# Kernel tuning notes

Hardware: AMD Instinct MI355X
Metric: run time of the kernel (lower is better)

The kernel has to match this reference:

```python
import jax, jax.numpy as jnp
import numpy as np

C = 256; COUT = 256; G = 8; GC = C // G; K = 3; P = K * K
PAD = 1; DIL = 1; STR = 1
EPS = 1e-5


def _group_norm(x, gamma, beta, groups=32, eps=EPS):
    # x: (N,H,W,C), torch.nn.GroupNorm semantics (biased var)
    N, H, W, Cc = x.shape
    xg = x.reshape(N, H, W, groups, Cc // groups)
    mu = xg.mean(axis=(1, 2, 4), keepdims=True)
    var = xg.var(axis=(1, 2, 4), keepdims=True)
    xg = (xg - mu) * jax.lax.rsqrt(var + eps)
    return xg.reshape(N, H, W, Cc) * gamma + beta


def _conv2d(x, w, b, stride=1, pad=1, groups=1):
    y = jax.lax.conv_general_dilated(
        x, w, (stride, stride), [(pad, pad), (pad, pad)],
        dimension_numbers=('NHWC', 'HWIO', 'NHWC'),
        feature_group_count=groups)
    return y + b


def _bilinear_gather(img, px, py, Hin, Win):
    x0 = jnp.floor(px); y0 = jnp.floor(py)
    wx1 = px - x0; wy1 = py - y0
    out = jnp.zeros(img.shape[:1] + px.shape[1:] + img.shape[-1:], img.dtype)
    for xi, wx in ((x0, 1.0 - wx1), (x0 + 1.0, wx1)):
        for yi, wy in ((y0, 1.0 - wy1), (y0 + 1.0, wy1)):
            valid = (xi >= 0) & (xi < Win) & (yi >= 0) & (yi < Hin)
            idx = (jnp.clip(yi, 0, Hin - 1) * Win + jnp.clip(xi, 0, Win - 1)).astype(jnp.int32)
            vals = jnp.take_along_axis(img, idx[..., None], axis=1)
            out = out + vals * (wx * wy * valid)[..., None]
    return out


def _forward(x, w_in, b_in, dw_w, dw_b, ln_g, ln_b, w_off, b_off, w_mask, b_mask,
             w_out, b_out, gn1_g, gn1_b, conv1_w, conv1_b, gn2_g, gn2_b,
             down_w, down_b, gn3_g, gn3_b):
    xs = jnp.transpose(x, (0, 2, 3, 1))  # NHWC
    N, H, W, _ = xs.shape
    # ---- DCNv3 ----
    x_proj = xs @ w_in + b_in                              # input_proj
    t = _conv2d(xs, dw_w, dw_b, stride=STR, pad=(K - 1) // 2, groups=C)  # depthwise
    mu = t.mean(-1, keepdims=True)
    var = t.var(-1, keepdims=True)
    t = (t - mu) * jax.lax.rsqrt(var + EPS) * ln_g + ln_b  # LayerNorm
    t = jax.nn.gelu(t, approximate=False)
    offset = (t @ w_off + b_off).reshape(N, H, W, G, P, 2)  # (x,y) pairs
    mask = jax.nn.softmax((t @ w_mask + b_mask).reshape(N, H, W, G, P), axis=-1)

    Hin, Win = H + 2 * PAD, W + 2 * PAD
    xp = jnp.pad(x_proj, ((0, 0), (PAD, PAD), (PAD, PAD), (0, 0)))
    base = (DIL * (K - 1)) // 2 + 0.5
    ref_y = (base + jnp.arange(H, dtype=xs.dtype) * STR) / Hin
    ref_x = (base + jnp.arange(W, dtype=xs.dtype) * STR) / Win
    ry, rx = jnp.meshgrid(ref_y, ref_x, indexing='ij')
    ref = jnp.stack([rx, ry], -1)[None, :, :, None, None, :]  # (1,H,W,1,1,2)
    d = jnp.arange(K, dtype=xs.dtype) * DIL - (DIL * (K - 1)) // 2
    gx, gy = jnp.meshgrid(d, d, indexing='ij')  # x varies fastest over axis0 (torch order)
    grid = jnp.stack([gx / Win, gy / Hin], -1).reshape(P, 2)
    spatial = jnp.array([Win, Hin], xs.dtype)
    loc = ref + grid + offset / spatial          # normalized [0,1], offset_scale=1
    px = loc[..., 0] * Win - 0.5                 # align_corners=False pixel coords
    py = loc[..., 1] * Hin - 0.5

    L = H * W
    img = xp.reshape(N, Hin * Win, G, GC).transpose(0, 2, 1, 3).reshape(N * G, Hin * Win, GC)
    pxf = jnp.transpose(px, (0, 3, 1, 2, 4)).reshape(N * G, L * P)
    pyf = jnp.transpose(py, (0, 3, 1, 2, 4)).reshape(N * G, L * P)
    sampled = _bilinear_gather(img, pxf, pyf, Hin, Win).reshape(N, G, L, P, GC)
    m = jnp.transpose(mask, (0, 3, 1, 2, 4)).reshape(N, G, L, P)
    agg = jnp.einsum('nglpc,nglp->nglc', sampled, m)
    y = agg.transpose(0, 2, 1, 3).reshape(N, H, W, C)
    y = y @ w_out + b_out                        # output_proj
    # ---- block_out ----
    y = jax.nn.silu(_group_norm(y, gn1_g, gn1_b))
    y = _conv2d(y, conv1_w, conv1_b, stride=1, pad=1)
    y = jax.nn.silu(_group_norm(y, gn2_g, gn2_b))
    # ---- down_sample ----
    y = _conv2d(y, down_w, down_b, stride=2, pad=1)
    y = _group_norm(y, gn3_g, gn3_b)
    return jnp.transpose(y, (0, 3, 1, 2))  # back to NCHW


def setup_inputs() -> dict:
    key = jax.random.key(0)
    ks = jax.random.split(key, 10)
    f = jnp.float32
    nrm = lambda k, shape, s: jax.random.normal(k, shape, dtype=f) * s
    N, H, W = 4, 64, 64
    return {
        'x': jax.random.normal(ks[0], (N, C, H, W), dtype=f),
        'w_in': nrm(ks[1], (C, C), 0.05), 'b_in': jnp.zeros((C,), f),
        'dw_w': nrm(ks[2], (K, K, 1, C), 0.1), 'dw_b': jnp.zeros((C,), f),
        'ln_g': jnp.ones((C,), f), 'ln_b': jnp.zeros((C,), f),
        'w_off': nrm(ks[3], (C, 2 * G * P), 0.02), 'b_off': nrm(ks[4], (2 * G * P,), 1.0),
        'w_mask': nrm(ks[5], (C, G * P), 0.02), 'b_mask': jnp.zeros((G * P,), f),
        'w_out': nrm(ks[6], (C, C), 0.05), 'b_out': jnp.zeros((C,), f),
        'gn1_g': jnp.ones((C,), f), 'gn1_b': jnp.zeros((C,), f),
        'conv1_w': nrm(ks[7], (3, 3, C, C), 0.02), 'conv1_b': jnp.zeros((C,), f),
        'gn2_g': jnp.ones((C,), f), 'gn2_b': jnp.zeros((C,), f),
        'down_w': nrm(ks[8], (3, 3, C, COUT), 0.02), 'down_b': jnp.zeros((COUT,), f),
        'gn3_g': jnp.ones((COUT,), f), 'gn3_b': jnp.zeros((COUT,), f),
    }


def reference(x, w_in, b_in, dw_w, dw_b, ln_g, ln_b, w_off, b_off, w_mask, b_mask,
              w_out, b_out, gn1_g, gn1_b, conv1_w, conv1_b, gn2_g, gn2_b,
              down_w, down_b, gn3_g, gn3_b):
    return _forward(x, w_in, b_in, dw_w, dw_b, ln_g, ln_b, w_off, b_off, w_mask,
                    b_mask, w_out, b_out, gn1_g, gn1_b, conv1_w, conv1_b,
                    gn2_g, gn2_b, down_w, down_b, gn3_g, gn3_b)
```

## Files before the change

### kernel.cpp

```cpp
#include <hip/hip_runtime.h>
#include <hip/hip_bf16.h>
#include <math.h>


typedef __attribute__((ext_vector_type(8))) short bf16x8;
typedef __attribute__((ext_vector_type(4))) float f32x4;

__device__ __forceinline__ float bf2f(unsigned short u){
  union { unsigned int i; float f; } v; v.i = ((unsigned int)u)<<16; return v.f;
}
__device__ __forceinline__ float blo(unsigned u){
  union { unsigned int i; float f; } v; v.i = u<<16; return v.f;
}
__device__ __forceinline__ float bhi(unsigned u){
  union { unsigned int i; float f; } v; v.i = u & 0xffff0000u; return v.f;
}
__device__ __forceinline__ unsigned short f2b(float f){
  __hip_bfloat16 h = __float2bfloat16(f);
  return *reinterpret_cast<unsigned short*>(&h);
}
__device__ __forceinline__ unsigned pk2(float lo, float hi){
  return (unsigned)f2b(lo) | ((unsigned)f2b(hi)<<16);
}

__device__ __forceinline__ void gload16(const void* g, void* l){
  auto gp = reinterpret_cast<const __attribute__((address_space(1))) uint32_t*>(
      reinterpret_cast<uintptr_t>(g));
  auto lp = reinterpret_cast<__attribute__((address_space(3))) uint32_t*>(
      reinterpret_cast<uintptr_t>(l));
  __builtin_amdgcn_global_load_lds(gp, lp, 16, 0, 0);
}

__global__ __launch_bounds__(256) void k_prep(
    const float* __restrict__ w_in, const float* __restrict__ w_out,
    const float* __restrict__ conv1_w, const float* __restrict__ down_w,
    const float* __restrict__ w_off, const float* __restrict__ w_mask,
    const float* __restrict__ b_off, const float* __restrict__ b_mask,
    __hip_bfloat16* __restrict__ w_inT, __hip_bfloat16* __restrict__ w_outT,
    __hip_bfloat16* __restrict__ c1T, __hip_bfloat16* __restrict__ dnT,
    __hip_bfloat16* __restrict__ w_omT, float* __restrict__ bias_om,
    float* __restrict__ stats, __hip_bfloat16* __restrict__ R3)
{
  int b = blockIdx.x;
  if (b < 160){
    __shared__ float tl[32][257];
    const float* W; __hip_bfloat16* WT; int Kd, kb;
    if (b < 8)      { W = w_in;    WT = w_inT;  Kd = 256;  kb = b; }
    else if (b <16) { W = w_out;   WT = w_outT; Kd = 256;  kb = b-8; }
    else if (b <88) { W = conv1_w; WT = c1T;    Kd = 2304; kb = b-16; }
    else            { W = down_w;  WT = dnT;    Kd = 2304; kb = b-88; }
    int k0 = kb*32;
    #pragma unroll
    for (int dk=0; dk<32; dk++) tl[dk][threadIdx.x] = W[(size_t)(k0+dk)*256 + threadIdx.x];
    __syncthreads();
    #pragma unroll
    for (int r=0; r<32; r++){
      int co = r*8 + (threadIdx.x>>5);
      int dk = threadIdx.x&31;
      WT[(size_t)co*Kd + k0 + dk] = __float2bfloat16(tl[dk][co]);
    }
  } else if (b < 416){
    int n = b - 160, k = threadIdx.x;
    float v = (n<144) ? w_off[(size_t)k*144 + n] : (n<216 ? w_mask[(size_t)k*72 + (n-144)] : 0.f);
    w_omT[(size_t)n*256 + k] = __float2bfloat16(v);
    if (k==0) bias_om[n] = (n<144) ? b_off[n] : (n<216 ? b_mask[n-144] : 0.f);
  } else if (b < 546){
    int gid = (b-416)*8 + (threadIdx.x>>5);
    if (gid >= 1040) return;
    int n = gid/260; int ci = gid - n*260;
    int r, c;
    if (ci < 66){ r = 0; c = ci; }
    else if (ci < 132){ r = 65; c = ci-66; }
    else { int q = ci-132; r = 1 + (q>>1); c = (q&1) ? 65 : 0; }
    uint4* p = (uint4*)(R3 + ((size_t)((n*66+r)*66+c))*256) + (threadIdx.x&31);
    *p = make_uint4(0,0,0,0);
  } else {
    stats[threadIdx.x] = 0.f;
    stats[256+threadIdx.x] = 0.f;
    stats[512+threadIdx.x] = 0.f;
  }
}

__global__ __launch_bounds__(256) void k_tr(const float* __restrict__ x, __hip_bfloat16* __restrict__ xs){
  __shared__ float tile[32][33];
  int n = blockIdx.z;
  int hw0 = blockIdx.x*32, c0 = blockIdx.y*32;
  int tx = threadIdx.x, ty = threadIdx.y;
  #pragma unroll
  for (int ii=0; ii<4; ii++){
    int ci = ty + ii*8;
    tile[ci][tx] = x[(size_t)(n*256 + c0+ci)*4096 + hw0 + tx];
  }
  __syncthreads();
  #pragma unroll
  for (int ii=0; ii<4; ii++){
    int hwi = ty + ii*8;
    xs[((size_t)n*4096 + hw0+hwi)*256 + c0 + tx] = __float2bfloat16(tile[tx][hwi]);
  }
}

template<int AMODE, int OMODE, int STRIDE, int KTOT, int NSHIFT>
__global__ __launch_bounds__(256) void k_mm(
    const __hip_bfloat16* __restrict__ A, const __hip_bfloat16* __restrict__ Bt,
    const float* __restrict__ bias, float* __restrict__ OF, __hip_bfloat16* __restrict__ OH,
    float* __restrict__ stats)
{
  constexpr int AROWS = 64;
  constexpr int MI = AROWS/32;
  constexpr int WROWS = AROWS/2;
  constexpr int JA = AROWS*128/4096;
  constexpr int BUFSZ = AROWS*128 + 16384;
  __shared__ uint4 lds4[2*BUFSZ/16];
  char* ldsc = (char*)lds4;
  const int tid = threadIdx.x;
  const int lane = tid & 63;
  const int wv = tid >> 6;
  const int wr = wv >> 1, wc = wv & 1;
  const int m0 = blockIdx.x * AROWS, n0 = blockIdx.y * 128;

  const int swz_s = ((tid >> 3) & 7) << 4;
  const int cby = ((tid & 7) << 4) ^ swz_s;
  const int kl = cby >> 1;
  int aoff[JA], boff[4];
  #pragma unroll
  for (int j=0;j<JA;j++){
    int row = j*32 + (tid>>3);
    if (AMODE==0){
      aoff[j] = (m0 + row) * KTOT + kl;
    } else {
      int m = m0 + row;
      int n, ho, wo;
      if (STRIDE==1){ n = m>>12; ho = (m>>6)&63; wo = m&63; }
      else          { n = m>>10; ho = (m>>5)&31; wo = m&31; }
      aoff[j] = ((n*66 + ho*STRIDE)*66 + wo*STRIDE)*256 + kl;
    }
  }
  #pragma unroll
  for (int j=0;j<4;j++) boff[j] = (n0 + j*32 + (tid>>3)) * KTOT + kl;
  char* ldsst = ldsc + wv*1024;

  const int fr = lane & 15;
  const int kb = (lane >> 4) << 4;
  const int swz_r = (fr & 7) << 4;
  int aRow[MI], bRow[4];
  #pragma unroll
  for (int i=0;i<MI;i++) aRow[i] = (wr*WROWS + i*16 + fr) * 128;
  #pragma unroll
  for (int i=0;i<4;i++)  bRow[i] = AROWS*128 + (wc*64 + i*16 + fr) * 128;
  int cb[2];
  cb[0] = kb ^ swz_r;
  cb[1] = (64 | kb) ^ swz_r;

  f32x4 acc[MI][4];
  #pragma unroll
  for (int mi=0;mi<MI;mi++)
    #pragma unroll
    for (int ni=0;ni<4;ni++)
      acc[mi][ni] = (f32x4){0.f,0.f,0.f,0.f};

  auto STAGE = [&](int buf, int t){
    const int k0 = t*64;
    int astep;
    if (AMODE==1){
      int tap = k0 >> 8;
      int kh = (tap>=6) ? 2 : (tap>=3 ? 1 : 0);
      int kw = tap - kh*3;
      astep = (kh*66 + kw)*256 + (k0 & 255);
    } else astep = k0;
    char* db = ldsst + buf*BUFSZ;
    #pragma unroll
    for (int j=0;j<JA;j++) gload16(A + aoff[j] + astep, db + j*4096);
    #pragma unroll
    for (int j=0;j<4;j++)  gload16(Bt + boff[j] + k0, db + AROWS*128 + j*4096);
  };

  constexpr int NT = KTOT / 64;
  STAGE(0, 0);
  __syncthreads();
  for (int t=0; t<NT; ++t){
    if (t+1 < NT) STAGE((t+1)&1, t+1);
    char* cbase = ldsc + (t&1)*BUFSZ;
    #pragma unroll
    for (int kk=0; kk<2; kk++){
      bf16x8 av[MI], bv[4];
      #pragma unroll
      for (int i=0;i<MI;i++) av[i] = *(const bf16x8*)(cbase + aRow[i] + cb[kk]);
      #pragma unroll
      for (int i=0;i<4;i++)  bv[i] = *(const bf16x8*)(cbase + bRow[i] + cb[kk]);
      #pragma unroll
      for (int mi=0;mi<MI;mi++)
        #pragma unroll
        for (int ni=0;ni<4;ni++)
          acc[mi][ni] = __builtin_amdgcn_mfma_f32_16x16x32_bf16(av[mi], bv[ni], acc[mi][ni], 0,0,0);
    }
    __syncthreads();
  }

  float bn[4];
  #pragma unroll
  for (int ni=0;ni<4;ni++) bn[ni] = bias[n0 + wc*64 + ni*16 + fr];
  float sni[4] = {0.f,0.f,0.f,0.f};
  float qni[4] = {0.f,0.f,0.f,0.f};
  #pragma unroll
  for (int mi=0;mi<MI;mi++){
    #pragma unroll
    for (int r=0;r<4;r++){
      int gr = m0 + wr*WROWS + mi*16 + (lane>>4)*4 + r;
      #pragma unroll
      for (int ni=0;ni<4;ni++){
        int gc = n0 + wc*64 + ni*16 + fr;
        float v = acc[mi][ni][r] + bn[ni];
        if (NSHIFT){ sni[ni] += v; qni[ni] += v*v; }
        if (OMODE==0){
          OF[(size_t)gr*256 + gc] = v;
        } else if (OMODE==1){
          int n = gr>>12, h = (gr>>6)&63, w = gr&63;
          OH[((size_t)((n*66)+(h+1))*66 + (w+1))*256 + gc] = __float2bfloat16(v);
        } else {
          if (gc < 216) OF[(size_t)gr*216 + gc] = v;
        }
      }
    }
  }
  if (NSHIFT){
    #pragma unroll
    for (int ni=0;ni<4;ni++){
      #pragma unroll
      for (int msk=16; msk<64; msk<<=1){
        sni[ni] += __shfl_xor(sni[ni], msk);
        qni[ni] += __shfl_xor(qni[ni], msk);
      }
      #pragma unroll
      for (int msk=1; msk<8; msk<<=1){
        sni[ni] += __shfl_xor(sni[ni], msk);
        qni[ni] += __shfl_xor(qni[ni], msk);
      }
    }
    float* ls = (float*)ldsc;
    if (tid < 32) ls[tid] = 0.f;
    __syncthreads();
    if ((lane & 7) == 0 && (lane & 48) == 0){
      int oct = (lane>>3) & 1;
      #pragma unroll
      for (int ni=0;ni<4;ni++){
        int idx = wc*8 + ni*2 + oct;
        atomicAdd(&ls[idx], sni[ni]);
        atomicAdd(&ls[16+idx], qni[ni]);
      }
    }
    __syncthreads();
    if (tid < 16){
      int gg = (m0>>NSHIFT)*32 + (n0>>3) + tid;
      atomicAdd(&stats[gg*2+0], ls[tid]);
      atomicAdd(&stats[gg*2+1], ls[16+tid]);
    }
  }
}

__global__ __launch_bounds__(256) void k_dwln(
    const __hip_bfloat16* __restrict__ xs, const float* __restrict__ dw_w, const float* __restrict__ dw_b,
    const float* __restrict__ ln_g, const float* __restrict__ ln_b, __hip_bfloat16* __restrict__ t)
{
  __shared__ float lw[9*256];
  __shared__ float lb[256], lg[256], lbt[256];
  int tid = threadIdx.x;
  #pragma unroll
  for (int p=0;p<9;p++) lw[p*256+tid] = dw_w[p*256+tid];
  lb[tid] = dw_b[tid]; lg[tid] = ln_g[tid]; lbt[tid] = ln_b[tid];
  __syncthreads();
  int posl = tid>>5, cg = tid&31, c0 = cg*8;
  int pos = blockIdx.x*8 + posl;
  int nb = pos>>12, h = (pos>>6)&63, w = pos&63;
  float v[8];
  #pragma unroll
  for (int k=0;k<8;k++) v[k] = lb[c0+k];
  #pragma unroll
  for (int kh=0;kh<3;kh++){
    int hin = h+kh-1;
    if (hin<0||hin>=64) continue;
    #pragma unroll
    for (int kw=0;kw<3;kw++){
      int win = w+kw-1;
      if (win<0||win>=64) continue;
      const unsigned short* xr = (const unsigned short*)xs + ((size_t)((nb*64+hin)*64+win))*256 + c0;
      uint4 u = *(const uint4*)xr;
      const float* wr = &lw[(kh*3+kw)*256 + c0];
      v[0] += blo(u.x)*wr[0]; v[1] += bhi(u.x)*wr[1];
      v[2] += blo(u.y)*wr[2]; v[3] += bhi(u.y)*wr[3];
      v[4] += blo(u.z)*wr[4]; v[5] += bhi(u.z)*wr[5];
      v[6] += blo(u.w)*wr[6]; v[7] += bhi(u.w)*wr[7];
    }
  }
  float s=0.f, s2=0.f;
  #pragma unroll
  for (int k=0;k<8;k++){ s += v[k]; s2 += v[k]*v[k]; }
  #pragma unroll
  for (int m=1;m<32;m<<=1){ s += __shfl_xor(s,m); s2 += __shfl_xor(s2,m); }
  float mu = s*(1.f/256.f);
  float var = s2*(1.f/256.f) - mu*mu;
  float rstd = rsqrtf(var + 1e-5f);
  float ge[8];
  #pragma unroll
  for (int k=0;k<8;k++){
    float xn = (v[k]-mu)*rstd*lg[c0+k] + lbt[c0+k];
    ge[k] = 0.5f*xn*(1.f + erff(xn*0.70710678118654752f));
  }
  uint4 o;
  o.x = pk2(ge[0],ge[1]); o.y = pk2(ge[2],ge[3]);
  o.z = pk2(ge[4],ge[5]); o.w = pk2(ge[6],ge[7]);
  *(uint4*)((unsigned short*)t + (size_t)pos*256 + c0) = o;
}

__global__ __launch_bounds__(256) void k_sample(
    const __hip_bfloat16* __restrict__ xp, const float* __restrict__ D, __hip_bfloat16* __restrict__ y)
{
  int tid = threadIdx.x;
  int pp = tid>>5;
  int g = (tid>>2)&7, li = tid&3;
  int pos = blockIdx.x*8 + pp;
  int nb = pos >> 12, h = (pos >> 6) & 63, w = pos & 63;
  const float* Dp = D + (size_t)pos*216;
  const float* offp = Dp + g*18;
  const float* mskp = Dp + 144 + g*9;
  float mr[9];
  #pragma unroll
  for (int p=0;p<9;p++) mr[p] = mskp[p];
  float mx = mr[0];
  #pragma unroll
  for (int p=1;p<9;p++) mx = fmaxf(mx, mr[p]);
  float ssum = 0.f;
  #pragma unroll
  for (int p=0;p<9;p++){ mr[p] = __expf(mr[p]-mx); ssum += mr[p]; }
  float rinv = 1.f/ssum;
  const unsigned short* img = (const unsigned short*)xp + (size_t)nb*4356*256 + g*32 + li*8;
  float a0=0,a1=0,a2=0,a3=0,a4=0,a5=0,a6=0,a7=0;
  #pragma unroll
  for (int p=0;p<9;p++){
    int di = p/3 - 1, dj = p%3 - 1;
    float2 off = *(const float2*)(offp + p*2);
    float px = (float)(w + 1 + di) + off.x;
    float py = (float)(h + 1 + dj) + off.y;
    float x0f = floorf(px), y0f = floorf(py);
    float wx1 = px - x0f, wy1 = py - y0f;
    float wx0 = 1.f - wx1, wy0 = 1.f - wy1;
    int x0 = (int)x0f, y0 = (int)y0f;
    float s0=0,s1=0,s2=0,s3=0,s4=0,s5=0,s6=0,s7=0;
    #pragma unroll
    for (int cy=0;cy<2;cy++){
      int yi = y0+cy;
      if (yi<0||yi>=66) continue;
      float wy = cy ? wy1 : wy0;
      #pragma unroll
      for (int cx=0;cx<2;cx++){
        int xi = x0+cx;
        if (xi<0||xi>=66) continue;
        float wq = (cx ? wx1 : wx0)*wy;
        uint4 u = *(const uint4*)(img + (size_t)(yi*66+xi)*256);
        s0 += blo(u.x)*wq; s1 += bhi(u.x)*wq;
        s2 += blo(u.y)*wq; s3 += bhi(u.y)*wq;
        s4 += blo(u.z)*wq; s5 += bhi(u.z)*wq;
        s6 += blo(u.w)*wq; s7 += bhi(u.w)*wq;
      }
    }
    float mp = mr[p]*rinv;
    a0 += s0*mp; a1 += s1*mp; a2 += s2*mp; a3 += s3*mp;
    a4 += s4*mp; a5 += s5*mp; a6 += s6*mp; a7 += s7*mp;
  }
  uint4 o;
  o.x = pk2(a0,a1); o.y = pk2(a2,a3); o.z = pk2(a4,a5); o.w = pk2(a6,a7);
  *(uint4*)((unsigned short*)y + (size_t)pos*256 + g*32 + li*8) = o;
}

__global__ __launch_bounds__(256) void k_gnapply(
    const float* __restrict__ X, const float* __restrict__ stats,
    const float* __restrict__ gamma, const float* __restrict__ beta,
    float* __restrict__ OF, __hip_bfloat16* __restrict__ OH,
    int nposshift, int do_silu, int outmode, int nmain)
{
  if ((int)blockIdx.x >= nmain){
    int gid = (blockIdx.x - nmain)*8 + (threadIdx.x>>5);
    if (gid >= 1040) return;
    int n = gid/260; int ci = gid - n*260;
    int r, c;
    if (ci < 66){ r = 0; c = ci; }
    else if (ci < 132){ r = 65; c = ci-66; }
    else { int q = ci-132; r = 1 + (q>>1); c = (q&1) ? 65 : 0; }
    uint4* p = (uint4*)(OH + ((size_t)((n*66+r)*66+c))*256) + (threadIdx.x&31);
    *p = make_uint4(0,0,0,0);
    return;
  }
  int idx = blockIdx.x*256 + threadIdx.x;
  int c = idx & 255;
  int row = idx >> 8;
  int nb = row >> nposshift;
  int p = row & ((1<<nposshift)-1);
  int grp = c >> 3;
  float S  = stats[(nb*32+grp)*2+0];
  float S2 = stats[(nb*32+grp)*2+1];
  float inv = 1.f / (float)(8 << nposshift);
  float mu = S*inv;
  float rs = rsqrtf(S2*inv - mu*mu + 1e-5f);
  float v = (X[idx] - mu) * rs * gamma[c] + beta[c];
  if (do_silu) v = v / (1.f + expf(-v));
  if (outmode == 1){
    int h = (row>>6)&63, w = row&63;
    OH[((size_t)((nb*66)+(h+1))*66 + (w+1))*256 + c] = __float2bfloat16(v);
  } else {
    OF[((size_t)(nb*256 + c) << nposshift) + p] = v;
  }
}

extern "C" void kernel_launch(void* const* d_in, const int* in_sizes, int n_in,
                              void* d_out, int out_size, void* d_ws, size_t ws_size,
                              hipStream_t stream) {
  const float* x      = (const float*)d_in[0];
  const float* w_in   = (const float*)d_in[1];
  const float* b_in   = (const float*)d_in[2];
  const float* dw_w   = (const float*)d_in[3];
  const float* dw_b   = (const float*)d_in[4];
  const float* ln_g   = (const float*)d_in[5];
  const float* ln_b   = (const float*)d_in[6];
  const float* w_off  = (const float*)d_in[7];
  const float* b_off  = (const float*)d_in[8];
  const float* w_mask = (const float*)d_in[9];
  const float* b_mask = (const float*)d_in[10];
  const float* w_out  = (const float*)d_in[11];
  const float* b_out  = (const float*)d_in[12];
  const float* gn1_g  = (const float*)d_in[13];
  const float* gn1_b  = (const float*)d_in[14];
  const float* conv1_w= (const float*)d_in[15];
  const float* conv1_b= (const float*)d_in[16];
  const float* gn2_g  = (const float*)d_in[17];
  const float* gn2_b  = (const float*)d_in[18];
  const float* down_w = (const float*)d_in[19];
  const float* down_b = (const float*)d_in[20];
  const float* gn3_g  = (const float*)d_in[21];
  const float* gn3_b  = (const float*)d_in[22];
  float* out = (float*)d_out;

  char* wsb = (char*)d_ws;
  float* R0 = (float*)wsb;
  float* R1 = (float*)(wsb + 16777216);
  __hip_bfloat16* R2 = (__hip_bfloat16*)(wsb + 33554432);
  __hip_bfloat16* R3 = (__hip_bfloat16*)(wsb + 41943040);
  __hip_bfloat16* R4 = (__hip_bfloat16*)(wsb + 50864128);
  char* R5 = wsb + 59785216;
  __hip_bfloat16* w_inT  = (__hip_bfloat16*)R5;
  __hip_bfloat16* w_outT = (__hip_bfloat16*)(R5 + 131072);
  __hip_bfloat16* w_omT  = (__hip_bfloat16*)(R5 + 262144);
  __hip_bfloat16* c1T    = (__hip_bfloat16*)(R5 + 393216);
  __hip_bfloat16* dnT    = (__hip_bfloat16*)(R5 + 1572864);
  float* bias_om         = (float*)(R5 + 2752512);
  float* stats           = (float*)(R5 + 2753536);

  k_prep<<<547, 256, 0, stream>>>(w_in, w_out, conv1_w, down_w, w_off, w_mask, b_off, b_mask,
                                  w_inT, w_outT, c1T, dnT, w_omT, bias_om, stats, R3);
  k_tr<<<dim3(128,8,4), dim3(32,8), 0, stream>>>(x, R2);
  k_mm<0,1,1,256,0><<<dim3(256,2), 256, 0, stream>>>(R2, w_inT, b_in, nullptr, R3, nullptr);
  k_dwln<<<2048, 256, 0, stream>>>(R2, dw_w, dw_b, ln_g, ln_b, R4);
  k_mm<0,2,1,256,0><<<dim3(256,2), 256, 0, stream>>>(R4, w_omT, bias_om, R1, nullptr, nullptr);
  k_sample<<<2048, 256, 0, stream>>>(R3, R1, R2);
  k_mm<0,0,1,256,12><<<dim3(256,2), 256, 0, stream>>>(R2, w_outT, b_out, R0, nullptr, stats);
  k_gnapply<<<16384+130, 256, 0, stream>>>(R0, stats, gn1_g, gn1_b, nullptr, R4, 12, 1, 1, 16384);
  k_mm<1,0,1,2304,12><<<dim3(256,2), 256, 0, stream>>>(R4, c1T, conv1_b, R1, nullptr, stats+256);
  k_gnapply<<<16384+130, 256, 0, stream>>>(R1, stats+256, gn2_g, gn2_b, nullptr, R3, 12, 1, 1, 16384);
  k_mm<1,0,2,2304,10><<<dim3(64,2), 256, 0, stream>>>(R3, dnT, down_b, R0, nullptr, stats+512);
  k_gnapply<<<4096, 256, 0, stream>>>(R0, stats+512, gn3_g, gn3_b, out, nullptr, 10, 0, 2, 4096);
}
```

Measured before the change: 262.7 us.

## Store GEMM outputs as bf16, vectorize GroupNorm apply, fold transpose into prep

GEMM outputs that feed GroupNorm are now stored as bf16 instead of fp32, which halves intermediate traffic. The GN apply kernel processes 8 channels per thread with vector loads and stores. The final GN gets a dedicated kernel that transposes through LDS to write NCHW output coalesced. The input transpose is merged into the prep kernel to remove a launch, and GEMM block IDs are remapped with an XCD-aware swizzle. The extra bf16 rounding before normalization adds a small precision risk.

```diff
diff --git a/kernel.cpp b/kernel.cpp
--- a/kernel.cpp
+++ b/kernel.cpp
@@ -6,9 +6,6 @@
 typedef __attribute__((ext_vector_type(8))) short bf16x8;
 typedef __attribute__((ext_vector_type(4))) float f32x4;
 
-__device__ __forceinline__ float bf2f(unsigned short u){
-  union { unsigned int i; float f; } v; v.i = ((unsigned int)u)<<16; return v.f;
-}
 __device__ __forceinline__ float blo(unsigned u){
   union { unsigned int i; float f; } v; v.i = u<<16; return v.f;
 }
@@ -32,6 +29,7 @@
 }
 
 __global__ __launch_bounds__(256) void k_prep(
+    const float* __restrict__ x,
     const float* __restrict__ w_in, const float* __restrict__ w_out,
     const float* __restrict__ conv1_w, const float* __restrict__ down_w,
     const float* __restrict__ w_off, const float* __restrict__ w_mask,
@@ -39,7 +37,8 @@
     __hip_bfloat16* __restrict__ w_inT, __hip_bfloat16* __restrict__ w_outT,
     __hip_bfloat16* __restrict__ c1T, __hip_bfloat16* __restrict__ dnT,
     __hip_bfloat16* __restrict__ w_omT, float* __restrict__ bias_om,
-    float* __restrict__ stats, __hip_bfloat16* __restrict__ R3)
+    float* __restrict__ stats, __hip_bfloat16* __restrict__ R3,
+    __hip_bfloat16* __restrict__ xs)
 {
   int b = blockIdx.x;
   if (b < 160){
@@ -74,28 +73,28 @@
     else { int q = ci-132; r = 1 + (q>>1); c = (q&1) ? 65 : 0; }
     uint4* p = (uint4*)(R3 + ((size_t)((n*66+r)*66+c))*256) + (threadIdx.x&31);
     *p = make_uint4(0,0,0,0);
-  } else {
+  } else if (b == 546){
     stats[threadIdx.x] = 0.f;
     stats[256+threadIdx.x] = 0.f;
     stats[512+threadIdx.x] = 0.f;
-  }
-}
-
-__global__ __launch_bounds__(256) void k_tr(const float* __restrict__ x, __hip_bfloat16* __restrict__ xs){
-  __shared__ float tile[32][33];
-  int n = blockIdx.z;
-  int hw0 = blockIdx.x*32, c0 = blockIdx.y*32;
-  int tx = threadIdx.x, ty = threadIdx.y;
-  #pragma unroll
-  for (int ii=0; ii<4; ii++){
-    int ci = ty + ii*8;
-    tile[ci][tx] = x[(size_t)(n*256 + c0+ci)*4096 + hw0 + tx];
-  }
-  __syncthreads();
-  #pragma unroll
-  for (int ii=0; ii<4; ii++){
-    int hwi = ty + ii*8;
-    xs[((size_t)n*4096 + hw0+hwi)*256 + c0 + tx] = __float2bfloat16(tile[tx][hwi]);
+  } else {
+    __shared__ float tile[32][33];
+    int t = b - 547;
+    int n = t >> 10;
+    int c0 = ((t >> 7) & 7) * 32;
+    int hw0 = (t & 127) * 32;
+    int tx = threadIdx.x & 31, ty = threadIdx.x >> 5;
+    #pragma unroll
+    for (int ii=0; ii<4; ii++){
+      int ci = ty + ii*8;
+      tile[ci][tx] = x[(size_t)(n*256 + c0+ci)*4096 + hw0 + tx];
+    }
+    __syncthreads();
+    #pragma unroll
+    for (int ii=0; ii<4; ii++){
+      int hwi = ty + ii*8;
+      xs[((size_t)n*4096 + hw0+hwi)*256 + c0 + tx] = __float2bfloat16(tile[tx][hwi]);
+    }
   }
 }
 
@@ -116,7 +115,11 @@
   const int lane = tid & 63;
   const int wv = tid >> 6;
   const int wr = wv >> 1, wc = wv & 1;
-  const int m0 = blockIdx.x * AROWS, n0 = blockIdx.y * 128;
+
+  int id = blockIdx.y * gridDim.x + blockIdx.x;
+  int cpx = (gridDim.x * gridDim.y) >> 3;
+  int sw = (id & 7) * cpx + (id >> 3);
+  const int m0 = (sw >> 1) * AROWS, n0 = (sw & 1) * 128;
 
   const int swz_s = ((tid >> 3) & 7) << 4;
   const int cby = ((tid & 7) << 4) ^ swz_s;
@@ -212,7 +215,7 @@
         float v = acc[mi][ni][r] + bn[ni];
         if (NSHIFT){ sni[ni] += v; qni[ni] += v*v; }
         if (OMODE==0){
-          OF[(size_t)gr*256 + gc] = v;
+          OH[(size_t)gr*256 + gc] = __float2bfloat16(v);
         } else if (OMODE==1){
           int n = gr>>12, h = (gr>>6)&63, w = gr&63;
           OH[((size_t)((n*66)+(h+1))*66 + (w+1))*256 + gc] = __float2bfloat16(v);
@@ -372,42 +375,79 @@
 }
 
 __global__ __launch_bounds__(256) void k_gnapply(
-    const float* __restrict__ X, const float* __restrict__ stats,
+    const __hip_bfloat16* __restrict__ X, const float* __restrict__ stats,
     const float* __restrict__ gamma, const float* __restrict__ beta,
-    float* __restrict__ OF, __hip_bfloat16* __restrict__ OH,
-    int nposshift, int do_silu, int outmode, int nmain)
+    __hip_bfloat16* __restrict__ OH, int nmain)
 {
-  if ((int)blockIdx.x >= nmain){
-    int gid = (blockIdx.x - nmain)*8 + (threadIdx.x>>5);
+  int b = blockIdx.x;
+  int tid = threadIdx.x;
+  if (b >= nmain){
+    int gid = (b - nmain)*8 + (tid>>5);
     if (gid >= 1040) return;
     int n = gid/260; int ci = gid - n*260;
     int r, c;
     if (ci < 66){ r = 0; c = ci; }
     else if (ci < 132){ r = 65; c = ci-66; }
     else { int q = ci-132; r = 1 + (q>>1); c = (q&1) ? 65 : 0; }
-    uint4* p = (uint4*)(OH + ((size_t)((n*66+r)*66+c))*256) + (threadIdx.x&31);
+    uint4* p = (uint4*)(OH + ((size_t)((n*66+r)*66+c))*256) + (tid&31);
     *p = make_uint4(0,0,0,0);
     return;
   }
-  int idx = blockIdx.x*256 + threadIdx.x;
-  int c = idx & 255;
-  int row = idx >> 8;
-  int nb = row >> nposshift;
-  int p = row & ((1<<nposshift)-1);
-  int grp = c >> 3;
+  int row = b*8 + (tid>>5);
+  int grp = tid & 31;
+  int c0 = grp*8;
+  int nb = row >> 12;
   float S  = stats[(nb*32+grp)*2+0];
   float S2 = stats[(nb*32+grp)*2+1];
-  float inv = 1.f / (float)(8 << nposshift);
+  const float inv = 1.f/32768.f;
   float mu = S*inv;
   float rs = rsqrtf(S2*inv - mu*mu + 1e-5f);
-  float v = (X[idx] - mu) * rs * gamma[c] + beta[c];
-  if (do_silu) v = v / (1.f + expf(-v));
-  if (outmode == 1){
-    int h = (row>>6)&63, w = row&63;
-    OH[((size_t)((nb*66)+(h+1))*66 + (w+1))*256 + c] = __float2bfloat16(v);
-  } else {
-    OF[((size_t)(nb*256 + c) << nposshift) + p] = v;
-  }
+  float4 g0 = *(const float4*)(gamma + c0), g1 = *(const float4*)(gamma + c0 + 4);
+  float4 bt0 = *(const float4*)(beta + c0), bt1 = *(const float4*)(beta + c0 + 4);
+  uint4 u = *(const uint4*)((const unsigned short*)X + (size_t)row*256 + c0);
+  float v[8] = { blo(u.x), bhi(u.x), blo(u.y), bhi(u.y), blo(u.z), bhi(u.z), blo(u.w), bhi(u.w) };
+  float gm[8] = { g0.x,g0.y,g0.z,g0.w,g1.x,g1.y,g1.z,g1.w };
+  float bb[8] = { bt0.x,bt0.y,bt0.z,bt0.w,bt1.x,bt1.y,bt1.z,bt1.w };
+  #pragma unroll
+  for (int k=0;k<8;k++){
+    float t = (v[k]-mu)*rs*gm[k] + bb[k];
+    v[k] = t / (1.f + expf(-t));
+  }
+  int h = (row>>6)&63, w = row&63;
+  uint4 o;
+  o.x = pk2(v[0],v[1]); o.y = pk2(v[2],v[3]); o.z = pk2(v[4],v[5]); o.w = pk2(v[6],v[7]);
+  *(uint4*)((unsigned short*)OH + ((size_t)((nb*66)+(h+1))*66 + (w+1))*256 + c0) = o;
+}
+
+__global__ __launch_bounds__(256) void k_gnout(
+    const __hip_bfloat16* __restrict__ X, const float* __restrict__ stats,
+    const float* __restrict__ gamma, const float* __restrict__ beta, float* __restrict__ out)
+{
+  __shared__ float val[8][1024];
+  int nb = blockIdx.x >> 5, cg = blockIdx.x & 31;
+  int c0 = cg*8;
+  float S  = stats[(nb*32+cg)*2+0];
+  float S2 = stats[(nb*32+cg)*2+1];
+  const float inv = 1.f/8192.f;
+  float mu = S*inv;
+  float rs = rsqrtf(S2*inv - mu*mu + 1e-5f);
+  float4 g0 = *(const float4*)(gamma + c0), g1 = *(const float4*)(gamma + c0 + 4);
+  float4 bt0 = *(const float4*)(beta + c0), bt1 = *(const float4*)(beta + c0 + 4);
+  float gm[8] = { g0.x,g0.y,g0.z,g0.w,g1.x,g1.y,g1.z,g1.w };
+  float bb[8] = { bt0.x,bt0.y,bt0.z,bt0.w,bt1.x,bt1.y,bt1.z,bt1.w };
+  #pragma unroll
+  for (int k=0;k<4;k++){
+    int pos = k*256 + threadIdx.x;
+    uint4 u = *(const uint4*)((const unsigned short*)X + ((size_t)(nb*1024+pos))*256 + c0);
+    float v[8] = { blo(u.x), bhi(u.x), blo(u.y), bhi(u.y), blo(u.z), bhi(u.z), blo(u.w), bhi(u.w) };
+    #pragma unroll
+    for (int q=0;q<8;q++) val[q][pos] = (v[q]-mu)*rs*gm[q] + bb[q];
+  }
+  __syncthreads();
+  int ch = threadIdx.x>>5, pl = threadIdx.x&31;
+  float* orow = out + (((size_t)(nb*256 + c0 + ch))<<10);
+  #pragma unroll
+  for (int j=0;j<32;j++) orow[pl + j*32] = val[ch][pl + j*32];
 }
 
 extern "C" void kernel_launch(void* const* d_in, const int* in_sizes, int n_in,
@@ -439,8 +479,9 @@
   float* out = (float*)d_out;
 
   char* wsb = (char*)d_ws;
-  float* R0 = (float*)wsb;
-  float* R1 = (float*)(wsb + 16777216);
+  __hip_bfloat16* R0h = (__hip_bfloat16*)wsb;
+  float* R1f = (float*)(wsb + 16777216);
+  __hip_bfloat16* R1h = (__hip_bfloat16*)(wsb + 16777216);
   __hip_bfloat16* R2 = (__hip_bfloat16*)(wsb + 33554432);
   __hip_bfloat16* R3 = (__hip_bfloat16*)(wsb + 41943040);
   __hip_bfloat16* R4 = (__hip_bfloat16*)(wsb + 50864128);
@@ -453,17 +494,16 @@
   float* bias_om         = (float*)(R5 + 2752512);
   float* stats           = (float*)(R5 + 2753536);
 
-  k_prep<<<547, 256, 0, stream>>>(w_in, w_out, conv1_w, down_w, w_off, w_mask, b_off, b_mask,
-                                  w_inT, w_outT, c1T, dnT, w_omT, bias_om, stats, R3);
-  k_tr<<<dim3(128,8,4), dim3(32,8), 0, stream>>>(x, R2);
+  k_prep<<<4643, 256, 0, stream>>>(x, w_in, w_out, conv1_w, down_w, w_off, w_mask, b_off, b_mask,
+                                   w_inT, w_outT, c1T, dnT, w_omT, bias_om, stats, R3, R2);
   k_mm<0,1,1,256,0><<<dim3(256,2), 256, 0, stream>>>(R2, w_inT, b_in, nullptr, R3, nullptr);
   k_dwln<<<2048, 256, 0, stream>>>(R2, dw_w, dw_b, ln_g, ln_b, R4);
-  k_mm<0,2,1,256,0><<<dim3(256,2), 256, 0, stream>>>(R4, w_omT, bias_om, R1, nullptr, nullptr);
-  k_sample<<<2048, 256, 0, stream>>>(R3, R1, R2);
-  k_mm<0,0,1,256,12><<<dim3(256,2), 256, 0, stream>>>(R2, w_outT, b_out, R0, nullptr, stats);
-  k_gnapply<<<16384+130, 256, 0, stream>>>(R0, stats, gn1_g, gn1_b, nullptr, R4, 12, 1, 1, 16384);
-  k_mm<1,0,1,2304,12><<<dim3(256,2), 256, 0, stream>>>(R4, c1T, conv1_b, R1, nullptr, stats+256);
-  k_gnapply<<<16384+130, 256, 0, stream>>>(R1, stats+256, gn2_g, gn2_b, nullptr, R3, 12, 1, 1, 16384);
-  k_mm<1,0,2,2304,10><<<dim3(64,2), 256, 0, stream>>>(R3, dnT, down_b, R0, nullptr, stats+512);
-  k_gnapply<<<4096, 256, 0, stream>>>(R0, stats+512, gn3_g, gn3_b, out, nullptr, 10, 0, 2, 4096);
-}
+  k_mm<0,2,1,256,0><<<dim3(256,2), 256, 0, stream>>>(R4, w_omT, bias_om, R1f, nullptr, nullptr);
+  k_sample<<<2048, 256, 0, stream>>>(R3, R1f, R2);
+  k_mm<0,0,1,256,12><<<dim3(256,2), 256, 0, stream>>>(R2, w_outT, b_out, nullptr, R0h, stats);
+  k_gnapply<<<2048+130, 256, 0, stream>>>(R0h, stats, gn1_g, gn1_b, R4, 2048);
+  k_mm<1,0,1,2304,12><<<dim3(256,2), 256, 0, stream>>>(R4, c1T, conv1_b, nullptr, R1h, stats+256);
+  k_gnapply<<<2048+130, 256, 0, stream>>>(R1h, stats+256, gn2_g, gn2_b, R3, 2048);
+  k_mm<1,0,2,2304,10><<<dim3(64,2), 256, 0, stream>>>(R3, dnT, down_b, nullptr, R0h, stats+512);
+  k_gnout<<<128, 256, 0, stream>>>(R0h, stats+512, gn3_g, gn3_b, out);
+}
```

New measurement: 246.7 us. 6.1% less time.
